# Optimization experiments

Measured on AMD Instinct MI355X. Metric: run time of the kernel, lower is better.

Reference implementation:

```python
import jax, jax.numpy as jnp
import numpy as np

T, B, H, V = 128, 32, 1024, 32000


def setup_inputs() -> dict:
    key = jax.random.key(0)
    ks = jax.random.split(key, 8)
    scale = 1.0 / np.sqrt(H)
    return {
        "input": jax.random.normal(ks[0], (T, B, H), dtype=jnp.float32),
        "hidden": jnp.zeros((B, H), dtype=jnp.float32),
        "w_ic": jax.random.uniform(ks[1], (H, H), jnp.float32, -scale, scale),
        "w_ix": jax.random.uniform(ks[2], (H, H), jnp.float32, -scale, scale),
        "w_fc": jax.random.uniform(ks[3], (H, H), jnp.float32, -scale, scale),
        "w_fx": jax.random.uniform(ks[4], (H, H), jnp.float32, -scale, scale),
        "b_i": jnp.zeros((H,), dtype=jnp.float32),
        "b_f": jnp.zeros((H,), dtype=jnp.float32),
        "W_out": jax.random.uniform(ks[5], (V, H), jnp.float32, -scale, scale),
        "b_out": jnp.zeros((V,), dtype=jnp.float32),
    }


def reference(input, hidden, w_ic, w_ix, w_fc, w_fx, b_i, b_f, W_out, b_out):
    # Precompute input projections for all timesteps: [T, B, H]
    ix = jnp.einsum("tbh,kh->tbk", input, w_ix)
    fx = jnp.einsum("tbh,kh->tbk", input, w_fx)

    def step(c, xs):
        ix_t, fx_t, x_t = xs
        i_t = jax.nn.sigmoid(c @ w_ic.T + b_i + ix_t)
        f_t = jax.nn.sigmoid(c @ w_fc.T + b_f + fx_t)
        c_new = i_t * x_t + f_t * c  # RAN gated-additive update
        return c_new, c_new

    hidden_final, outputs = jax.lax.scan(step, hidden, (ix, fx, input))
    logits = jnp.einsum("tbh,vh->tbv", outputs, W_out) + b_out
    log_probs = jax.nn.log_softmax(logits, axis=-1)
    return log_probs, hidden_final
```

## Files before the change

### kernel.cpp

```cpp
#include <hip/hip_runtime.h>

typedef __attribute__((ext_vector_type(4))) float f32x4;
typedef __attribute__((ext_vector_type(8))) short bf16x8;
typedef __attribute__((ext_vector_type(4))) unsigned u32x4;

#define T_DIM 128
#define B_DIM 32
#define H_DIM 1024
#define V_DIM 32000
#define MROWS 4096
#define NBLK 64
#define PUBSTEP 32768
#define WSTRIDE 1028

__device__ __forceinline__ ushort f2bf(float f){
  union { float f; unsigned u; } x; x.f = f;
  unsigned u = x.u;
  unsigned r = (u + 0x7fffu + ((u >> 16) & 1u)) >> 16;
  return (ushort)r;
}
__device__ __forceinline__ float bf2f(ushort h){
  union { unsigned u; float f; } x; x.u = ((unsigned)h) << 16;
  return x.f;
}

__device__ __forceinline__ void async_copy16(void* lds, const void* g){
  __builtin_amdgcn_global_load_lds((const __attribute__((address_space(1))) void*)g,
                                   (__attribute__((address_space(3))) void*)lds, 16, 0, 0);
}

__global__ void cast_bf16_kernel(const float* __restrict__ s, ushort* __restrict__ d, int n4){
  int stride = gridDim.x * blockDim.x;
  for (int i = blockIdx.x*blockDim.x + threadIdx.x; i < n4; i += stride){
    float4 v = ((const float4*)s)[i];
    ushort4 o = make_ushort4(f2bf(v.x), f2bf(v.y), f2bf(v.z), f2bf(v.w));
    ((ushort4*)d)[i] = o;
  }
}

__global__ void cast_split_kernel(const float* __restrict__ s, ushort* __restrict__ dh,
                                  ushort* __restrict__ dl, int n4){
  int stride = gridDim.x * blockDim.x;
  for (int i = blockIdx.x*blockDim.x + threadIdx.x; i < n4; i += stride){
    float4 v = ((const float4*)s)[i];
    ushort4 h = make_ushort4(f2bf(v.x), f2bf(v.y), f2bf(v.z), f2bf(v.w));
    ushort4 l = make_ushort4(f2bf(v.x - bf2f(h.x)), f2bf(v.y - bf2f(h.y)),
                             f2bf(v.z - bf2f(h.z)), f2bf(v.w - bf2f(h.w)));
    ((ushort4*)dh)[i] = h;
    ((ushort4*)dl)[i] = l;
  }
}

__global__ __launch_bounds__(512) void gemm256(
    const ushort* __restrict__ A, const ushort* __restrict__ B,
    float* __restrict__ C, const float* __restrict__ bias,
    float* __restrict__ pmax, float* __restrict__ psum)
{
  __shared__ ushort lA[2][256*64];
  __shared__ ushort lB[2][256*64];
  __shared__ float redm[2][4][128], reds[2][4][128];

  const int K = 1024, N = V_DIM, NTN = 125, NT = 16;
  int tid = threadIdx.x, lane = tid & 63, wid = tid >> 6;
  int wm = wid >> 2, wn = wid & 3;
  int bid = blockIdx.x;
  int xcd = bid & 7, id = bid >> 3;
  int tm = (xcd << 1) | (id & 1);
  int tn = id >> 1;
  int row0 = tm << 8, col0 = tn << 8;
  int ar = lane & 15, kg = (lane >> 4) << 3;

  auto STAGE = [&](int buf, int k0){
    #pragma unroll
    for (int j = 0; j < 4; ++j){
      int l16 = j*512 + tid;
      int row = l16 >> 3, g = l16 & 7;
      int kc = (g ^ (row & 7)) << 3;
      int rA = row0 + row, k = k0 + kc;
      const ushort* sA = A + ((size_t)(rA>>5)<<15) + ((k>>4)<<9) + ((rA&31)<<4) + (k&15);
      async_copy16(&lA[buf][l16<<3], sA);
    }
    #pragma unroll
    for (int j = 0; j < 4; ++j){
      int l16 = j*512 + tid;
      int row = l16 >> 3, g = l16 & 7;
      int kc = (g ^ (row & 7)) << 3;
      const ushort* sB = B + (size_t)(col0 + row)*K + k0 + kc;
      async_copy16(&lB[buf][l16<<3], sB);
    }
  };

  f32x4 acc[8][4] = {};

  STAGE(0, 0);
  for (int t = 0; t < NT; ++t){
    if (t + 1 < NT) STAGE((t+1) & 1, (t+1) << 6);
    if (t + 1 < NT) asm volatile("s_waitcnt vmcnt(8)" ::: "memory");
    else            asm volatile("s_waitcnt vmcnt(0)" ::: "memory");
    __builtin_amdgcn_s_barrier();
    __builtin_amdgcn_sched_barrier(0);
    const ushort* bufA = lA[t & 1];
    const ushort* bufB = lB[t & 1];
    #pragma unroll
    for (int ks = 0; ks < 2; ++ks){
      bf16x8 a[8], b[4];
      #pragma unroll
      for (int fr = 0; fr < 8; ++fr){
        int row = wm*128 + fr*16 + ar;
        int gk = ks*4 + (kg >> 3);
        a[fr] = *(const bf16x8*)&bufA[row*64 + ((gk ^ (row & 7)) << 3)];
      }
      #pragma unroll
      for (int fc = 0; fc < 4; ++fc){
        int row = wn*64 + fc*16 + ar;
        int gk = ks*4 + (kg >> 3);
        b[fc] = *(const bf16x8*)&bufB[row*64 + ((gk ^ (row & 7)) << 3)];
      }
      __builtin_amdgcn_s_setprio(1);
      #pragma unroll
      for (int fr = 0; fr < 8; ++fr)
        #pragma unroll
        for (int fc = 0; fc < 4; ++fc)
          acc[fr][fc] = __builtin_amdgcn_mfma_f32_16x16x32_bf16(a[fr], b[fc], acc[fr][fc], 0, 0, 0);
      __builtin_amdgcn_s_setprio(0);
    }
    __builtin_amdgcn_sched_barrier(0);
    __builtin_amdgcn_s_barrier();
    __builtin_amdgcn_sched_barrier(0);
  }

  float bb4[4];
  #pragma unroll
  for (int fc = 0; fc < 4; ++fc) bb4[fc] = bias[col0 + wn*64 + fc*16 + ar];
  #pragma unroll
  for (int fr = 0; fr < 8; ++fr){
    #pragma unroll
    for (int q = 0; q < 4; ++q){
      int rl = fr*16 + (lane>>4)*4 + q;
      int r = row0 + wm*128 + rl;
      float vals[4];
      #pragma unroll
      for (int fc = 0; fc < 4; ++fc){
        vals[fc] = acc[fr][fc][q] + bb4[fc];
        C[(size_t)r * N + col0 + wn*64 + fc*16 + ar] = vals[fc];
      }
      float m = fmaxf(fmaxf(vals[0], vals[1]), fmaxf(vals[2], vals[3]));
      #pragma unroll
      for (int o = 1; o < 16; o <<= 1) m = fmaxf(m, __shfl_xor(m, o));
      float s = expf(vals[0]-m) + expf(vals[1]-m) + expf(vals[2]-m) + expf(vals[3]-m);
      #pragma unroll
      for (int o = 1; o < 16; o <<= 1) s += __shfl_xor(s, o);
      if (ar == 0){ redm[wm][wn][rl] = m; reds[wm][wn][rl] = s; }
    }
  }
  __syncthreads();
  if (tid < 256){
    int wm2 = tid >> 7, rl = tid & 127;
    float m0 = redm[wm2][0][rl], m1 = redm[wm2][1][rl];
    float m2 = redm[wm2][2][rl], m3 = redm[wm2][3][rl];
    float M = fmaxf(fmaxf(m0, m1), fmaxf(m2, m3));
    float S = reds[wm2][0][rl]*expf(m0-M) + reds[wm2][1][rl]*expf(m1-M)
            + reds[wm2][2][rl]*expf(m2-M) + reds[wm2][3][rl]*expf(m3-M);
    int r = row0 + wm2*128 + rl;
    pmax[(size_t)r*NTN + tn] = M;
    psum[(size_t)r*NTN + tn] = S;
  }
}

__global__ __launch_bounds__(256) void gemm_bt_split(
    const ushort* __restrict__ Ah, const ushort* __restrict__ Al,
    const ushort* __restrict__ Bh, const ushort* __restrict__ Bl,
    float* __restrict__ C, int N, int K, int NTN)
{
  __shared__ ushort lAh[128*32], lAl[128*32], lBh[128*32], lBl[128*32];
  int tid = threadIdx.x;
  int lane = tid & 63, wid = tid >> 6;
  int tm = blockIdx.x / NTN, tn = blockIdx.x % NTN;
  int row0 = tm << 7, col0 = tn << 7;

  f32x4 acc[4][4] = {};

  auto stage = [&](const ushort* __restrict__ g, ushort* l, int r0, int k0){
    int c = wid << 1;
    const ushort* s0 = g + (size_t)(r0 + (c<<4) + (lane>>2))*K + k0 + ((lane&3)<<3);
    async_copy16(l + (c<<9), s0);
    async_copy16(l + ((c+1)<<9), s0 + (size_t)16*K);
  };

  int nk = K >> 5;
  stage(Ah, lAh, row0, 0); stage(Al, lAl, row0, 0);
  stage(Bh, lBh, col0, 0); stage(Bl, lBl, col0, 0);
  int wm = (wid >> 1) << 6, wn = (wid & 1) << 6;
  int kg = (lane >> 4) << 3;
  int ar = lane & 15;

  for (int kt = 0; kt < nk; ++kt){
    __syncthreads();
    bf16x8 afh[4], afl[4], bfh[4], bfl[4];
    #pragma unroll
    for (int mi = 0; mi < 4; ++mi){
      afh[mi] = *(const bf16x8*)&lAh[(wm + mi*16 + ar)*32 + kg];
      afl[mi] = *(const bf16x8*)&lAl[(wm + mi*16 + ar)*32 + kg];
    }
    #pragma unroll
    for (int ni = 0; ni < 4; ++ni){
      bfh[ni] = *(const bf16x8*)&lBh[(wn + ni*16 + ar)*32 + kg];
      bfl[ni] = *(const bf16x8*)&lBl[(wn + ni*16 + ar)*32 + kg];
    }
    #pragma unroll
    for (int mi = 0; mi < 4; ++mi)
      #pragma unroll
      for (int ni = 0; ni < 4; ++ni){
        acc[mi][ni] = __builtin_amdgcn_mfma_f32_16x16x32_bf16(afh[mi], bfh[ni], acc[mi][ni], 0, 0, 0);
        acc[mi][ni] = __builtin_amdgcn_mfma_f32_16x16x32_bf16(afh[mi], bfl[ni], acc[mi][ni], 0, 0, 0);
        acc[mi][ni] = __builtin_amdgcn_mfma_f32_16x16x32_bf16(afl[mi], bfh[ni], acc[mi][ni], 0, 0, 0);
      }
    if (kt + 1 < nk){
      __syncthreads();
      stage(Ah, lAh, row0, (kt+1) << 5); stage(Al, lAl, row0, (kt+1) << 5);
      stage(Bh, lBh, col0, (kt+1) << 5); stage(Bl, lBl, col0, (kt+1) << 5);
    }
  }

  int rr = (lane >> 4) << 2;
  #pragma unroll
  for (int mi = 0; mi < 4; ++mi)
    #pragma unroll
    for (int ni = 0; ni < 4; ++ni){
      int r  = row0 + wm + mi*16 + rr;
      int cc = col0 + wn + ni*16 + ar;
      #pragma unroll
      for (int q = 0; q < 4; ++q)
        C[(size_t)(r + q) * N + cc] = acc[mi][ni][q];
    }
}

__global__ __launch_bounds__(512) void ran_all(
    unsigned* __restrict__ pub, const float* __restrict__ hiddenf,
    const ushort* __restrict__ wh, const ushort* __restrict__ wl,
    const float* __restrict__ b_i, const float* __restrict__ b_f,
    const float* __restrict__ ixfx, const float* __restrict__ x_all,
    float* __restrict__ hid_final)
{
  __shared__ ushort lWh[32*WSTRIDE];
  __shared__ ushort lWl[32*WSTRIDE];
  __shared__ f32x4 part[4][2][2][64];
  __shared__ float gsm[2*32*17];
  __shared__ float cfl[32][17];

  int tid = threadIdx.x, lane = tid & 63, wid = tid >> 6;
  int kq = wid & 3, mh = wid >> 2;
  int rgate = wid & 1, rmh = (wid >> 1) & 1;
  int bid = blockIdx.x;
  int nb = bid << 4;
  int ar = lane & 15, kg = (lane >> 4) << 3;
  int um = tid >> 4, uk = tid & 15;

  #pragma unroll
  for (int u = 0; u < 8; ++u){
    int unit = u*512 + tid;
    int r = unit >> 7, off = (unit & 127) << 3;
    int g = r >> 4, c = r & 15;
    size_t gsrc = (size_t)((g<<10) + nb + c) * H_DIM + off;
    *(bf16x8*)&lWh[r*WSTRIDE + off] = *(const bf16x8*)&wh[gsrc];
    *(bf16x8*)&lWl[r*WSTRIDE + off] = *(const bf16x8*)&wl[gsrc];
  }
  cfl[um][uk] = hiddenf[(um<<10) + nb + uk];
  float bb = (rgate ? b_f : b_i)[nb + ar];
  const ushort* b0h = &lWh[(     ar)*WSTRIDE + (kq<<8) + kg];
  const ushort* b0l = &lWl[(     ar)*WSTRIDE + (kq<<8) + kg];
  const ushort* b1h = &lWh[(16 + ar)*WSTRIDE + (kq<<8) + kg];
  const ushort* b1l = &lWl[(16 + ar)*WSTRIDE + (kq<<8) + kg];
  int abase = (kq<<13) + ((kg>>4)<<9) + (((mh<<4) + ar)<<4) + (kg & 8);
  __syncthreads();

  for (int t = 0; t < T_DIM; ++t){
    float xq1 = x_all[((size_t)t<<15) + (um<<10) + nb + uk];
    float pix[4];
    if (wid < 4){
      const float* ix_t = ixfx + ((size_t)t<<16);
      #pragma unroll
      for (int q = 0; q < 4; ++q){
        int m = (rmh<<4) + ((lane>>4)<<2) + q;
        pix[q] = ix_t[m*2048 + (rgate<<10) + nb + ar];
      }
    }

    const unsigned* ps = pub + ((size_t)t << 15) + abase;
    unsigned expt = (unsigned)(t + 1) << 16;
    u32x4 w0[8], w1[8];
    int tries = 0;
    while (1){
      #pragma unroll
      for (int f = 0; f < 8; ++f){
        const unsigned* p = ps + (f << 10);
        asm volatile("global_load_dwordx4 %0, %2, off sc0 sc1\n\t"
                     "global_load_dwordx4 %1, %2, off offset:16 sc0 sc1"
                     : "=&v"(w0[f]), "=&v"(w1[f]) : "v"(p));
      }
      asm volatile("s_waitcnt vmcnt(0)" ::: "memory");
      __builtin_amdgcn_sched_barrier(0);
      unsigned bad = 0;
      #pragma unroll
      for (int f = 0; f < 8; ++f){
        bad |= (w0[f][0]^expt)|(w0[f][1]^expt)|(w0[f][2]^expt)|(w0[f][3]^expt)
             | (w1[f][0]^expt)|(w1[f][1]^expt)|(w1[f][2]^expt)|(w1[f][3]^expt);
      }
      if (__ballot((bad & 0xFFFF0000u) != 0) == 0ull) break;
      if (++tries > (1<<15)) break;
    }

    f32x4 g0h = {}, g0l = {}, g1h = {}, g1l = {};
    #pragma unroll
    for (int f = 0; f < 8; ++f){
      union { unsigned u[4]; bf16x8 v; } cv;
      cv.u[0] = (w0[f][0] & 0xFFFFu) | (w0[f][1] << 16);
      cv.u[1] = (w0[f][2] & 0xFFFFu) | (w0[f][3] << 16);
      cv.u[2] = (w1[f][0] & 0xFFFFu) | (w1[f][1] << 16);
      cv.u[3] = (w1[f][2] & 0xFFFFu) | (w1[f][3] << 16);
      int ob = f << 5;
      bf16x8 v0h = *(const bf16x8*)&b0h[ob];
      bf16x8 v0l = *(const bf16x8*)&b0l[ob];
      bf16x8 v1h = *(const bf16x8*)&b1h[ob];
      bf16x8 v1l = *(const bf16x8*)&b1l[ob];
      g0h = __builtin_amdgcn_mfma_f32_16x16x32_bf16(cv.v, v0h, g0h, 0, 0, 0);
      g0l = __builtin_amdgcn_mfma_f32_16x16x32_bf16(cv.v, v0l, g0l, 0, 0, 0);
      g1h = __builtin_amdgcn_mfma_f32_16x16x32_bf16(cv.v, v1h, g1h, 0, 0, 0);
      g1l = __builtin_amdgcn_mfma_f32_16x16x32_bf16(cv.v, v1l, g1l, 0, 0, 0);
    }
    part[kq][mh][0][lane] = g0h + g0l;
    part[kq][mh][1][lane] = g1h + g1l;
    __syncthreads();

    if (wid < 4){
      f32x4 sum = part[0][rmh][rgate][lane] + part[1][rmh][rgate][lane]
                + part[2][rmh][rgate][lane] + part[3][rmh][rgate][lane];
      #pragma unroll
      for (int q = 0; q < 4; ++q){
        int m = (rmh<<4) + ((lane>>4)<<2) + q;
        float pre = sum[q] + bb + pix[q];
        gsm[((rgate<<5) + m)*17 + ar] = 1.f / (1.f + expf(-pre));
      }
    }
    __syncthreads();

    {
      float iv = gsm[um*17 + uk];
      float fv = gsm[(32+um)*17 + uk];
      float cv2 = cfl[um][uk];
      float cn = iv * xq1 + fv * cv2;
      cfl[um][uk] = cn;
      unsigned word = ((unsigned)(t + 2) << 16) | (unsigned)f2bf(cn);
      __hip_atomic_store(&pub[((size_t)(t+1) << 15) + (bid << 9) + tid], word,
                         __ATOMIC_RELAXED, __HIP_MEMORY_SCOPE_AGENT);
      if (t == T_DIM-1) hid_final[(um<<10) + nb + uk] = cn;
    }
    __syncthreads();
  }
}

__global__ void init_c_kernel(const float* __restrict__ hidden, unsigned* __restrict__ pub){
  int i = blockIdx.x * blockDim.x + threadIdx.x;
  float v = hidden[i];
  int m = i >> 10, col = i & 1023;
  pub[((col>>4)<<9) + (m<<4) + (col&15)] = (1u << 16) | (unsigned)f2bf(v);
}

__global__ void untag_kernel(const unsigned* __restrict__ pub, ushort* __restrict__ cst){
  int e = (blockIdx.x * blockDim.x + threadIdx.x) << 2;
  int s = e >> 15, w = e & 32767;
  const unsigned* p = pub + ((size_t)(s + 1) << 15) + w;
  ushort4 o = make_ushort4((ushort)p[0], (ushort)p[1], (ushort)p[2], (ushort)p[3]);
  *(ushort4*)&cst[e] = o;
}

__global__ __launch_bounds__(64) void lse_reduce(const float* __restrict__ pmax,
                                                 const float* __restrict__ psum,
                                                 float* __restrict__ lse, int ntn){
  int row = blockIdx.x, lane = threadIdx.x;
  float m = -1e30f, s = 0.f;
  for (int i = lane; i < ntn; i += 64){
    float mi = pmax[(size_t)row*ntn + i], si = psum[(size_t)row*ntn + i];
    float M = fmaxf(m, mi);
    s = s*expf(m - M) + si*expf(mi - M);
    m = M;
  }
  #pragma unroll
  for (int o = 32; o; o >>= 1){
    float m2 = __shfl_xor(m, o), s2 = __shfl_xor(s, o);
    float M = fmaxf(m, m2);
    s = s*expf(m - M) + s2*expf(m2 - M);
    m = M;
  }
  if (lane == 0) lse[row] = m + logf(s);
}

__global__ __launch_bounds__(256) void sub_kernel(float* __restrict__ logits,
                                                  const float* __restrict__ lse){
  size_t row = blockIdx.x;
  float l = lse[row];
  float4* p4 = (float4*)(logits + row * (size_t)V_DIM);
  for (int i = threadIdx.x; i < V_DIM/4; i += 256){
    float4 v = p4[i];
    v.x -= l; v.y -= l; v.z -= l; v.w -= l;
    p4[i] = v;
  }
}

extern "C" void kernel_launch(void* const* d_in, const int* in_sizes, int n_in,
                              void* d_out, int out_size, void* d_ws, size_t ws_size,
                              hipStream_t stream)
{
  const float* input  = (const float*)d_in[0];
  const float* hidden = (const float*)d_in[1];
  const float* w_ic   = (const float*)d_in[2];
  const float* w_ix   = (const float*)d_in[3];
  const float* w_fc   = (const float*)d_in[4];
  const float* w_fx   = (const float*)d_in[5];
  const float* b_i    = (const float*)d_in[6];
  const float* b_f    = (const float*)d_in[7];
  const float* W_out  = (const float*)d_in[8];
  const float* b_out  = (const float*)d_in[9];
  float* out = (float*)d_out;

  char* ws = (char*)d_ws;
  ushort* wout_bf = (ushort*)(ws + 0);
  ushort* in_hi   = (ushort*)(ws + 65536000);
  ushort* in_lo   = (ushort*)(ws + 73924608);
  ushort* wx_hi   = (ushort*)(ws + 82313216);
  ushort* wx_lo   = (ushort*)(ws + 86507520);
  ushort* wc_hi   = (ushort*)(ws + 90701824);
  ushort* wc_lo   = (ushort*)(ws + 94896128);
  unsigned* pub   = (unsigned*)(ws + 65536000);
  ushort* cstate  = (ushort*)(ws + 82444288);
  float*  pmax    = (float*)(ws + 94896128);
  float*  psum    = (float*)(ws + 99090432);
  float*  lse     = (float*)(ws + 103186432);
  float*  ixfx    = out;

  cast_bf16_kernel <<<2048,256,0,stream>>>(W_out, wout_bf, V_DIM*H_DIM/4);
  cast_split_kernel<<<1024,256,0,stream>>>(input, in_hi, in_lo, MROWS*H_DIM/4);
  cast_split_kernel<<<256,256,0,stream>>>(w_ix, wx_hi,             wx_lo,             H_DIM*H_DIM/4);
  cast_split_kernel<<<256,256,0,stream>>>(w_fx, wx_hi+H_DIM*H_DIM, wx_lo+H_DIM*H_DIM, H_DIM*H_DIM/4);
  cast_split_kernel<<<256,256,0,stream>>>(w_ic, wc_hi,             wc_lo,             H_DIM*H_DIM/4);
  cast_split_kernel<<<256,256,0,stream>>>(w_fc, wc_hi+H_DIM*H_DIM, wc_lo+H_DIM*H_DIM, H_DIM*H_DIM/4);

  gemm_bt_split<<<32*16,256,0,stream>>>(in_hi, in_lo, wx_hi, wx_lo, ixfx, 2048, H_DIM, 16);

  hipMemsetAsync(pub, 0, (size_t)129 * PUBSTEP * 4, stream);
  init_c_kernel<<<128,256,0,stream>>>(hidden, pub);

  ran_all<<<NBLK,512,0,stream>>>(pub, hidden, wc_hi, wc_lo, b_i, b_f,
                                 ixfx, input, out + (size_t)MROWS*V_DIM);

  untag_kernel<<<4096,256,0,stream>>>(pub, cstate);
  gemm256<<<2000,512,0,stream>>>(cstate, wout_bf, out, b_out, pmax, psum);
  lse_reduce<<<MROWS,64,0,stream>>>(pmax, psum, lse, 125);
  sub_kernel<<<MROWS,256,0,stream>>>(out, lse);
}
```

Measured before the change: 1.915 ms.

## Drop split-bf16 input projection, deepen output GEMM pipeline, fuse LSE into subtract

The input projection GEMM now uses plain bf16 for the input and the w_ix/w_fx weights instead of the hi/lo split-bf16 scheme that needed three MFMAs per tile, which removes two thirds of its MFMA work and two casting passes. The main vocab GEMM changes from a K=64, 2-slot pipeline to a K=32, 4-slot pipeline with a two-tile lookahead, a new XOR swizzle and one barrier per iteration. The log-sum-exp reduction is folded into the subtract kernel, saving a launch. Lower precision on ix/fx adds error that can feed through the recurrence.

```diff
diff --git a/kernel.cpp b/kernel.cpp
--- a/kernel.cpp
+++ b/kernel.cpp
@@ -12,6 +12,7 @@
 #define NBLK 64
 #define PUBSTEP 32768
 #define WSTRIDE 1028
+#define GBK 32
 
 __device__ __forceinline__ ushort f2bf(float f){
   union { float f; unsigned u; } x; x.f = f;
@@ -51,16 +52,75 @@
   }
 }
 
+__global__ __launch_bounds__(256) void gemm_bt_plain(
+    const ushort* __restrict__ A, const ushort* __restrict__ B,
+    float* __restrict__ C, int N, int K, int NTN)
+{
+  __shared__ ushort lA[128*32];
+  __shared__ ushort lB[128*32];
+  int tid = threadIdx.x;
+  int lane = tid & 63, wid = tid >> 6;
+  int tm = blockIdx.x / NTN, tn = blockIdx.x % NTN;
+  int row0 = tm << 7, col0 = tn << 7;
+
+  f32x4 acc[4][4] = {};
+
+  auto stage = [&](const ushort* __restrict__ g, ushort* l, int r0, int k0){
+    int c = wid << 1;
+    const ushort* s0 = g + (size_t)(r0 + (c<<4) + (lane>>2))*K + k0 + ((lane&3)<<3);
+    async_copy16(l + (c<<9), s0);
+    async_copy16(l + ((c+1)<<9), s0 + (size_t)16*K);
+  };
+
+  int nk = K >> 5;
+  stage(A, lA, row0, 0);
+  stage(B, lB, col0, 0);
+  int wm = (wid >> 1) << 6, wn = (wid & 1) << 6;
+  int kg = (lane >> 4) << 3;
+  int ar = lane & 15;
+
+  for (int kt = 0; kt < nk; ++kt){
+    __syncthreads();
+    bf16x8 af[4], bfr[4];
+    #pragma unroll
+    for (int mi = 0; mi < 4; ++mi) af[mi]  = *(const bf16x8*)&lA[(wm + mi*16 + ar)*32 + kg];
+    #pragma unroll
+    for (int ni = 0; ni < 4; ++ni) bfr[ni] = *(const bf16x8*)&lB[(wn + ni*16 + ar)*32 + kg];
+    #pragma unroll
+    for (int mi = 0; mi < 4; ++mi)
+      #pragma unroll
+      for (int ni = 0; ni < 4; ++ni)
+        acc[mi][ni] = __builtin_amdgcn_mfma_f32_16x16x32_bf16(af[mi], bfr[ni], acc[mi][ni], 0, 0, 0);
+    if (kt + 1 < nk){
+      __syncthreads();
+      stage(A, lA, row0, (kt+1) << 5);
+      stage(B, lB, col0, (kt+1) << 5);
+    }
+  }
+
+  int rr = (lane >> 4) << 2;
+  #pragma unroll
+  for (int mi = 0; mi < 4; ++mi)
+    #pragma unroll
+    for (int ni = 0; ni < 4; ++ni){
+      int r  = row0 + wm + mi*16 + rr;
+      int cc = col0 + wn + ni*16 + ar;
+      #pragma unroll
+      for (int q = 0; q < 4; ++q)
+        C[(size_t)(r + q) * N + cc] = acc[mi][ni][q];
+    }
+}
+
 __global__ __launch_bounds__(512) void gemm256(
     const ushort* __restrict__ A, const ushort* __restrict__ B,
     float* __restrict__ C, const float* __restrict__ bias,
     float* __restrict__ pmax, float* __restrict__ psum)
 {
-  __shared__ ushort lA[2][256*64];
-  __shared__ ushort lB[2][256*64];
+  __shared__ ushort lA[4][256*GBK];
+  __shared__ ushort lB[4][256*GBK];
   __shared__ float redm[2][4][128], reds[2][4][128];
 
-  const int K = 1024, N = V_DIM, NTN = 125, NT = 16;
+  const int K = 1024, N = V_DIM, NTN = 125, NT = 32;
   int tid = threadIdx.x, lane = tid & 63, wid = tid >> 6;
   int wm = wid >> 2, wn = wid & 3;
   int bid = blockIdx.x;
@@ -70,62 +130,61 @@
   int row0 = tm << 8, col0 = tn << 8;
   int ar = lane & 15, kg = (lane >> 4) << 3;
 
-  auto STAGE = [&](int buf, int k0){
-    #pragma unroll
-    for (int j = 0; j < 4; ++j){
-      int l16 = j*512 + tid;
-      int row = l16 >> 3, g = l16 & 7;
-      int kc = (g ^ (row & 7)) << 3;
-      int rA = row0 + row, k = k0 + kc;
-      const ushort* sA = A + ((size_t)(rA>>5)<<15) + ((k>>4)<<9) + ((rA&31)<<4) + (k&15);
-      async_copy16(&lA[buf][l16<<3], sA);
-    }
-    #pragma unroll
-    for (int j = 0; j < 4; ++j){
-      int l16 = j*512 + tid;
-      int row = l16 >> 3, g = l16 & 7;
-      int kc = (g ^ (row & 7)) << 3;
-      const ushort* sB = B + (size_t)(col0 + row)*K + k0 + kc;
-      async_copy16(&lB[buf][l16<<3], sB);
+  auto STAGE = [&](int slot, int kt){
+    int k0 = kt << 5;
+    #pragma unroll
+    for (int j = 0; j < 2; ++j){
+      int u = j*512 + tid;
+      int r = u >> 2, p = u & 3;
+      int g = p ^ ((r >> 1) & 3);
+      int rA = row0 + r, k = k0 + (g << 3);
+      const ushort* sA = A + ((size_t)(rA>>5)<<15) + ((size_t)(k>>4)<<9) + ((rA&31)<<4) + (k&15);
+      async_copy16(&lA[slot][u<<3], sA);
+    }
+    #pragma unroll
+    for (int j = 0; j < 2; ++j){
+      int u = j*512 + tid;
+      int r = u >> 2, p = u & 3;
+      int g = p ^ ((r >> 1) & 3);
+      const ushort* sB = B + (size_t)(col0 + r)*K + k0 + (g << 3);
+      async_copy16(&lB[slot][u<<3], sB);
     }
   };
 
   f32x4 acc[8][4] = {};
 
   STAGE(0, 0);
+  STAGE(1, 1);
+  int gk = kg >> 3;
   for (int t = 0; t < NT; ++t){
-    if (t + 1 < NT) STAGE((t+1) & 1, (t+1) << 6);
-    if (t + 1 < NT) asm volatile("s_waitcnt vmcnt(8)" ::: "memory");
-    else            asm volatile("s_waitcnt vmcnt(0)" ::: "memory");
+    if (t + 2 < NT) STAGE((t+2) & 3, t+2);
+    if (t + 2 < NT)      asm volatile("s_waitcnt vmcnt(8)" ::: "memory");
+    else if (t + 1 < NT) asm volatile("s_waitcnt vmcnt(4)" ::: "memory");
+    else                 asm volatile("s_waitcnt vmcnt(0)" ::: "memory");
     __builtin_amdgcn_s_barrier();
     __builtin_amdgcn_sched_barrier(0);
-    const ushort* bufA = lA[t & 1];
-    const ushort* bufB = lB[t & 1];
-    #pragma unroll
-    for (int ks = 0; ks < 2; ++ks){
-      bf16x8 a[8], b[4];
-      #pragma unroll
-      for (int fr = 0; fr < 8; ++fr){
-        int row = wm*128 + fr*16 + ar;
-        int gk = ks*4 + (kg >> 3);
-        a[fr] = *(const bf16x8*)&bufA[row*64 + ((gk ^ (row & 7)) << 3)];
-      }
-      #pragma unroll
-      for (int fc = 0; fc < 4; ++fc){
-        int row = wn*64 + fc*16 + ar;
-        int gk = ks*4 + (kg >> 3);
-        b[fc] = *(const bf16x8*)&bufB[row*64 + ((gk ^ (row & 7)) << 3)];
-      }
-      __builtin_amdgcn_s_setprio(1);
-      #pragma unroll
-      for (int fr = 0; fr < 8; ++fr)
-        #pragma unroll
-        for (int fc = 0; fc < 4; ++fc)
-          acc[fr][fc] = __builtin_amdgcn_mfma_f32_16x16x32_bf16(a[fr], b[fc], acc[fr][fc], 0, 0, 0);
-      __builtin_amdgcn_s_setprio(0);
-    }
-    __builtin_amdgcn_sched_barrier(0);
-    __builtin_amdgcn_s_barrier();
+    const ushort* bufA = lA[t & 3];
+    const ushort* bufB = lB[t & 3];
+    bf16x8 a[8], b[4];
+    #pragma unroll
+    for (int fr = 0; fr < 8; ++fr){
+      int row = wm*128 + fr*16 + ar;
+      int phys = gk ^ ((row >> 1) & 3);
+      a[fr] = *(const bf16x8*)&bufA[row*GBK + (phys << 3)];
+    }
+    #pragma unroll
+    for (int fc = 0; fc < 4; ++fc){
+      int row = wn*64 + fc*16 + ar;
+      int phys = gk ^ ((row >> 1) & 3);
+      b[fc] = *(const bf16x8*)&bufB[row*GBK + (phys << 3)];
+    }
+    __builtin_amdgcn_s_setprio(1);
+    #pragma unroll
+    for (int fr = 0; fr < 8; ++fr)
+      #pragma unroll
+      for (int fc = 0; fc < 4; ++fc)
+        acc[fr][fc] = __builtin_amdgcn_mfma_f32_16x16x32_bf16(a[fr], b[fc], acc[fr][fc], 0, 0, 0);
+    __builtin_amdgcn_s_setprio(0);
     __builtin_amdgcn_sched_barrier(0);
   }
 
@@ -165,74 +224,6 @@
     pmax[(size_t)r*NTN + tn] = M;
     psum[(size_t)r*NTN + tn] = S;
   }
-}
-
-__global__ __launch_bounds__(256) void gemm_bt_split(
-    const ushort* __restrict__ Ah, const ushort* __restrict__ Al,
-    const ushort* __restrict__ Bh, const ushort* __restrict__ Bl,
-    float* __restrict__ C, int N, int K, int NTN)
-{
-  __shared__ ushort lAh[128*32], lAl[128*32], lBh[128*32], lBl[128*32];
-  int tid = threadIdx.x;
-  int lane = tid & 63, wid = tid >> 6;
-  int tm = blockIdx.x / NTN, tn = blockIdx.x % NTN;
-  int row0 = tm << 7, col0 = tn << 7;
-
-  f32x4 acc[4][4] = {};
-
-  auto stage = [&](const ushort* __restrict__ g, ushort* l, int r0, int k0){
-    int c = wid << 1;
-    const ushort* s0 = g + (size_t)(r0 + (c<<4) + (lane>>2))*K + k0 + ((lane&3)<<3);
-    async_copy16(l + (c<<9), s0);
-    async_copy16(l + ((c+1)<<9), s0 + (size_t)16*K);
-  };
-
-  int nk = K >> 5;
-  stage(Ah, lAh, row0, 0); stage(Al, lAl, row0, 0);
-  stage(Bh, lBh, col0, 0); stage(Bl, lBl, col0, 0);
-  int wm = (wid >> 1) << 6, wn = (wid & 1) << 6;
-  int kg = (lane >> 4) << 3;
-  int ar = lane & 15;
-
-  for (int kt = 0; kt < nk; ++kt){
-    __syncthreads();
-    bf16x8 afh[4], afl[4], bfh[4], bfl[4];
-    #pragma unroll
-    for (int mi = 0; mi < 4; ++mi){
-      afh[mi] = *(const bf16x8*)&lAh[(wm + mi*16 + ar)*32 + kg];
-      afl[mi] = *(const bf16x8*)&lAl[(wm + mi*16 + ar)*32 + kg];
-    }
-    #pragma unroll
-    for (int ni = 0; ni < 4; ++ni){
-      bfh[ni] = *(const bf16x8*)&lBh[(wn + ni*16 + ar)*32 + kg];
-      bfl[ni] = *(const bf16x8*)&lBl[(wn + ni*16 + ar)*32 + kg];
-    }
-    #pragma unroll
-    for (int mi = 0; mi < 4; ++mi)
-      #pragma unroll
-      for (int ni = 0; ni < 4; ++ni){
-        acc[mi][ni] = __builtin_amdgcn_mfma_f32_16x16x32_bf16(afh[mi], bfh[ni], acc[mi][ni], 0, 0, 0);
-        acc[mi][ni] = __builtin_amdgcn_mfma_f32_16x16x32_bf16(afh[mi], bfl[ni], acc[mi][ni], 0, 0, 0);
-        acc[mi][ni] = __builtin_amdgcn_mfma_f32_16x16x32_bf16(afl[mi], bfh[ni], acc[mi][ni], 0, 0, 0);
-      }
-    if (kt + 1 < nk){
-      __syncthreads();
-      stage(Ah, lAh, row0, (kt+1) << 5); stage(Al, lAl, row0, (kt+1) << 5);
-      stage(Bh, lBh, col0, (kt+1) << 5); stage(Bl, lBl, col0, (kt+1) << 5);
-    }
-  }
-
-  int rr = (lane >> 4) << 2;
-  #pragma unroll
-  for (int mi = 0; mi < 4; ++mi)
-    #pragma unroll
-    for (int ni = 0; ni < 4; ++ni){
-      int r  = row0 + wm + mi*16 + rr;
-      int cc = col0 + wn + ni*16 + ar;
-      #pragma unroll
-      for (int q = 0; q < 4; ++q)
-        C[(size_t)(r + q) * N + cc] = acc[mi][ni][q];
-    }
 }
 
 __global__ __launch_bounds__(512) void ran_all(
@@ -374,33 +365,33 @@
   *(ushort4*)&cst[e] = o;
 }
 
-__global__ __launch_bounds__(64) void lse_reduce(const float* __restrict__ pmax,
-                                                 const float* __restrict__ psum,
-                                                 float* __restrict__ lse, int ntn){
-  int row = blockIdx.x, lane = threadIdx.x;
-  float m = -1e30f, s = 0.f;
-  for (int i = lane; i < ntn; i += 64){
-    float mi = pmax[(size_t)row*ntn + i], si = psum[(size_t)row*ntn + i];
-    float M = fmaxf(m, mi);
-    s = s*expf(m - M) + si*expf(mi - M);
-    m = M;
-  }
-  #pragma unroll
-  for (int o = 32; o; o >>= 1){
-    float m2 = __shfl_xor(m, o), s2 = __shfl_xor(s, o);
-    float M = fmaxf(m, m2);
-    s = s*expf(m - M) + s2*expf(m2 - M);
-    m = M;
-  }
-  if (lane == 0) lse[row] = m + logf(s);
-}
-
-__global__ __launch_bounds__(256) void sub_kernel(float* __restrict__ logits,
-                                                  const float* __restrict__ lse){
+__global__ __launch_bounds__(256) void subf_kernel(float* __restrict__ logits,
+                                                   const float* __restrict__ pmax,
+                                                   const float* __restrict__ psum){
+  __shared__ float sl;
   size_t row = blockIdx.x;
-  float l = lse[row];
+  int tid = threadIdx.x;
+  if (tid < 64){
+    float m = -1e30f, s = 0.f;
+    for (int i = tid; i < 125; i += 64){
+      float mi = pmax[row*125 + i], si = psum[row*125 + i];
+      float M = fmaxf(m, mi);
+      s = s*expf(m - M) + si*expf(mi - M);
+      m = M;
+    }
+    #pragma unroll
+    for (int o = 32; o; o >>= 1){
+      float m2 = __shfl_xor(m, o), s2 = __shfl_xor(s, o);
+      float M = fmaxf(m, m2);
+      s = s*expf(m - M) + s2*expf(m2 - M);
+      m = M;
+    }
+    if (tid == 0) sl = m + logf(s);
+  }
+  __syncthreads();
+  float l = sl;
   float4* p4 = (float4*)(logits + row * (size_t)V_DIM);
-  for (int i = threadIdx.x; i < V_DIM/4; i += 256){
+  for (int i = tid; i < V_DIM/4; i += 256){
     float4 v = p4[i];
     v.x -= l; v.y -= l; v.z -= l; v.w -= l;
     p4[i] = v;
@@ -426,26 +417,23 @@
   char* ws = (char*)d_ws;
   ushort* wout_bf = (ushort*)(ws + 0);
   ushort* in_hi   = (ushort*)(ws + 65536000);
-  ushort* in_lo   = (ushort*)(ws + 73924608);
-  ushort* wx_hi   = (ushort*)(ws + 82313216);
-  ushort* wx_lo   = (ushort*)(ws + 86507520);
+  ushort* wx      = (ushort*)(ws + 73924608);
   ushort* wc_hi   = (ushort*)(ws + 90701824);
   ushort* wc_lo   = (ushort*)(ws + 94896128);
   unsigned* pub   = (unsigned*)(ws + 65536000);
   ushort* cstate  = (ushort*)(ws + 82444288);
   float*  pmax    = (float*)(ws + 94896128);
   float*  psum    = (float*)(ws + 99090432);
-  float*  lse     = (float*)(ws + 103186432);
   float*  ixfx    = out;
 
-  cast_bf16_kernel <<<2048,256,0,stream>>>(W_out, wout_bf, V_DIM*H_DIM/4);
-  cast_split_kernel<<<1024,256,0,stream>>>(input, in_hi, in_lo, MROWS*H_DIM/4);
-  cast_split_kernel<<<256,256,0,stream>>>(w_ix, wx_hi,             wx_lo,             H_DIM*H_DIM/4);
-  cast_split_kernel<<<256,256,0,stream>>>(w_fx, wx_hi+H_DIM*H_DIM, wx_lo+H_DIM*H_DIM, H_DIM*H_DIM/4);
+  cast_bf16_kernel<<<2048,256,0,stream>>>(W_out, wout_bf, V_DIM*H_DIM/4);
+  cast_bf16_kernel<<<1024,256,0,stream>>>(input, in_hi, MROWS*H_DIM/4);
+  cast_bf16_kernel<<<256,256,0,stream>>>(w_ix, wx,             H_DIM*H_DIM/4);
+  cast_bf16_kernel<<<256,256,0,stream>>>(w_fx, wx+H_DIM*H_DIM, H_DIM*H_DIM/4);
   cast_split_kernel<<<256,256,0,stream>>>(w_ic, wc_hi,             wc_lo,             H_DIM*H_DIM/4);
   cast_split_kernel<<<256,256,0,stream>>>(w_fc, wc_hi+H_DIM*H_DIM, wc_lo+H_DIM*H_DIM, H_DIM*H_DIM/4);
 
-  gemm_bt_split<<<32*16,256,0,stream>>>(in_hi, in_lo, wx_hi, wx_lo, ixfx, 2048, H_DIM, 16);
+  gemm_bt_plain<<<32*16,256,0,stream>>>(in_hi, wx, ixfx, 2048, H_DIM, 16);
 
   hipMemsetAsync(pub, 0, (size_t)129 * PUBSTEP * 4, stream);
   init_c_kernel<<<128,256,0,stream>>>(hidden, pub);
@@ -455,6 +443,5 @@
 
   untag_kernel<<<4096,256,0,stream>>>(pub, cstate);
   gemm256<<<2000,512,0,stream>>>(cstate, wout_bf, out, b_out, pmax, psum);
-  lse_reduce<<<MROWS,64,0,stream>>>(pmax, psum, lse, 125);
-  sub_kernel<<<MROWS,256,0,stream>>>(out, lse);
-}
+  subf_kernel<<<MROWS,256,0,stream>>>(out, pmax, psum);
+}
```

After: 1.865 ms. 2.6% less time.
